# Performance work log

Hardware: AMD Instinct MI355X
Metric: run time of the kernel (lower is better)

The kernel has to match this reference:

```python
import jax, jax.numpy as jnp
import numpy as np

DT = 0.01  # init kwarg dt
M = 501    # microstructure feature length (hardcoded split [501, 501] in source)
H = 128    # hidden width


def _mlp(x, W1, b1, W2, b2):
    # Linear -> Softplus -> Linear
    return jax.nn.softplus(x @ W1 + b1) @ W2 + b2


def _linear_init(key, fan_in, fan_out):
    k1, k2 = jax.random.split(key)
    s = 1.0 / np.sqrt(fan_in)
    W = jax.random.uniform(k1, (fan_in, fan_out), minval=-s, maxval=s, dtype=jnp.float32)
    b = jax.random.uniform(k2, (fan_out,), minval=-s, maxval=s, dtype=jnp.float32)
    return W, b


def setup_inputs() -> dict:
    key = jax.random.key(0)
    ks = jax.random.split(key, 10)
    B, T = 32768, 512
    Ew1, Eb1 = _linear_init(ks[0], 2 * M, H)   # energy net: Linear(1002,128)
    Ew2, Eb2 = _linear_init(ks[1], H, 1)
    nw1, nb1 = _linear_init(ks[2], M, H)       # nu net: Linear(501,128)
    nw2, nb2 = _linear_init(ks[3], H, 1)
    bw1, bb1 = _linear_init(ks[4], 2 * M, H)   # beta net: Linear(1002,128)
    bw2, bb2 = _linear_init(ks[5], H, 1)
    e = jax.random.normal(ks[6], (B, T, 1), dtype=jnp.float32) * 0.01
    e_dot = jax.random.normal(ks[7], (B, T, 1), dtype=jnp.float32) * 0.01
    E = jax.random.uniform(ks[8], (B, M), dtype=jnp.float32)
    nu = jax.random.uniform(ks[9], (B, M), dtype=jnp.float32)
    return dict(e=e, e_dot=e_dot, E=E, nu=nu,
                Ew1=Ew1, Eb1=Eb1, Ew2=Ew2, Eb2=Eb2,
                nw1=nw1, nb1=nb1, nw2=nw2, nb2=nb2,
                bw1=bw1, bb1=bb1, bw2=bw2, bb2=bb2)


def reference(e, e_dot, E, nu,
              Ew1, Eb1, Ew2, Eb2,
              nw1, nb1, nw2, nb2,
              bw1, bb1, bw2, bb2):
    # microstructure encoder: m = concat(E, nu) -> [B, 1002]; constant over time,
    # so the three small MLPs are evaluated ONCE (the per-step autograd.grad of the
    # quadratic energy/dissipation potentials has closed form).
    m = jnp.concatenate((E, nu), axis=-1)
    Emod = jnp.exp(_mlp(m, Ew1, Eb1, Ew2, Eb2))                              # exp(E(m))    [B,1]
    nu_feat = m[:, M:]                                                        # second half of split
    nuv = jnp.exp(jnp.square(_mlp(nu_feat, nw1, nb1, nw2, nb2)) / 40000.0)    # exp(nu(.))   [B,1]
    beta = jnp.square(_mlp(m, bw1, bb1, bw2, bb2)) / 40000.0                  # beta(m)      [B,1]

    # Per-step closed-form derivatives of
    #   energy    = 1/2 exp(E(m)) u^2 + 1/2 (u - v)^2        (u = e_t, v = xi_t)
    #   potential = -1/2 exp(nu) p^2 + 1/2 sum(beta q^2)     (p = e_dot_t, q = -dE/dv = e_t - xi_t)
    #   s_eq = exp(E) u + (u - v);  s_neq = dPhi/dp = -exp(nu) p;  kinetics = dPhi/dq = beta q
    def step(xi, inputs):
        et, edt = inputs                     # [B,1] each
        q = et - xi
        stress_t = Emod * et + q + nuv * edt  # s_eq - s_neq
        xi_next = xi + DT * beta * q
        return xi_next, (stress_t, xi)

    xi0 = jnp.zeros_like(e[:, 0])            # [B,1]
    eT = jnp.moveaxis(e, 1, 0)               # [T,B,1]
    edT = jnp.moveaxis(e_dot, 1, 0)
    _, (stress, xi) = jax.lax.scan(step, xi0, (eT, edT))
    return jnp.moveaxis(stress, 0, 1), jnp.moveaxis(xi, 0, 1)  # [B,T,1] each
```

## Files before the change

### kernel.cpp

```cpp
#include <hip/hip_runtime.h>
#include <hip/hip_bf16.h>

#define M_ 501
#define T_ 512
#define DT_ 0.01f

typedef __attribute__((ext_vector_type(8))) __bf16 bf16x8;
typedef __attribute__((ext_vector_type(4))) float f32x4;

static __device__ __forceinline__ unsigned int pack2(float a, float b) {
    __hip_bfloat16 ha = __float2bfloat16(a);
    __hip_bfloat16 hb = __float2bfloat16(b);
    unsigned short ua = __builtin_bit_cast(unsigned short, ha);
    unsigned short ub = __builtin_bit_cast(unsigned short, hb);
    return (unsigned int)ua | ((unsigned int)ub << 16);
}

__global__ void build_w(const float* __restrict__ Ew1, const float* __restrict__ bw1,
                        const float* __restrict__ nw1, __hip_bfloat16* __restrict__ Wswz) {
    int idx = blockIdx.x * 256 + threadIdx.x;
    if (idx >= 32 * 24 * 64 * 8) return;
    int e  = idx & 7;
    int l  = (idx >> 3) & 63;
    int t  = idx >> 9;
    int nt = t % 24, k0 = t / 24;
    int k  = k0 * 32 + ((l >> 4) << 3) + e;
    int n  = nt * 16 + (l & 15);
    float v = 0.f;
    if (n < 128)      { if (k < 2*M_)             v = Ew1[k * 128 + n]; }
    else if (n < 256) { if (k < 2*M_)             v = bw1[k * 128 + (n - 128)]; }
    else              { if (k >= M_ && k < 2*M_)  v = nw1[(k - M_) * 128 + (n - 256)]; }
    Wswz[idx] = __float2bfloat16(v);
}

__global__ __launch_bounds__(512, 2) void fused_all(
    const float* __restrict__ E, const float* __restrict__ nu,
    const __hip_bfloat16* __restrict__ Wswz,
    const float* __restrict__ Eb1, const float* __restrict__ bb1, const float* __restrict__ nb1,
    const float* __restrict__ Ew2, const float* __restrict__ bw2, const float* __restrict__ nw2,
    const float* __restrict__ Eb2, const float* __restrict__ bb2, const float* __restrict__ nb2,
    const float* __restrict__ e, const float* __restrict__ ed,
    float* __restrict__ stress, float* __restrict__ xiout, int B)
{
    const int tid = threadIdx.x;
    const int wid = tid >> 6, l = tid & 63;
    const int c = l & 15, g = l >> 4;
    const int brow = blockIdx.x * 64;

    __shared__ __align__(16) unsigned char sAraw[3][64 * 128];
    __shared__ float cb1[384], cw2[384];
    __shared__ float lds_s[3][64];

    if (tid < 384) {
        int n = tid;
        cb1[n] = (n < 128) ? Eb1[n] : (n < 256) ? bb1[n - 128] : nb1[n - 256];
        cw2[n] = (n < 128) ? Ew2[n] : (n < 256) ? bw2[n - 128] : nw2[n - 256];
    }
    if (tid < 192) ((float*)lds_s)[tid] = 0.f;

    const int sr = tid >> 3, su = tid & 7;
    const size_t rb = (size_t)(brow + sr) * M_;
    f32x4 qa0, qa1, qa2, qb0, qb1, qb2; int oa = 0, ob = 0;

    auto stage_load = [&](int ch, f32x4& r0, f32x4& r1, f32x4& r2, int& ro) {
        int cu = ch * 8 + su;
        bool slow = (cu == 62) | (cu >= 124);
        if (!slow) {
            const float* src = (cu < 62) ? E : nu;
            int off = (cu < 62) ? cu * 8 : cu * 8 - M_;
            size_t s = rb + (size_t)off;
            ro = (int)(s & 3);
            const f32x4* p = (const f32x4*)(src + (s & ~(size_t)3));
            r0 = p[0]; r1 = p[1]; r2 = p[2];
        } else {
            int kb = cu * 8;
            auto ldx = [&](int k) -> float {
                return (k < M_) ? E[rb + k] : ((k < 2 * M_) ? nu[rb + k - M_] : 0.f);
            };
            r0 = (f32x4){ldx(kb+0), ldx(kb+1), ldx(kb+2), ldx(kb+3)};
            r1 = (f32x4){ldx(kb+4), ldx(kb+5), ldx(kb+6), ldx(kb+7)};
            r2 = (f32x4){0.f, 0.f, 0.f, 0.f};
            ro = 0;
        }
    };
    auto stage_finish = [&](int nbuf, f32x4& r0, f32x4& r1, f32x4& r2, int& ro) {
        asm volatile("" : "+v"(r0), "+v"(r1), "+v"(r2));
        float g0=r0[0], g1=r0[1], g2=r0[2], g3=r0[3],
              g4=r1[0], g5=r1[1], g6=r1[2], g7=r1[3],
              g8=r2[0], g9=r2[1], g10=r2[2];
        const bool o2 = (ro & 2) != 0, o1 = (ro & 1) != 0;
        float u0 = o2?g2:g0, u1 = o2?g3:g1, u2 = o2?g4:g2, u3 = o2?g5:g3,
              u4 = o2?g6:g4, u5 = o2?g7:g5, u6 = o2?g8:g6, u7 = o2?g9:g7,
              u8 = o2?g10:g8;
        float f0 = o1?u1:u0, f1 = o1?u2:u1, f2 = o1?u3:u2, f3 = o1?u4:u3,
              f4 = o1?u5:u4, f5 = o1?u6:u5, f6 = o1?u7:u6, f7 = o1?u8:u7;
        uint4 vv;
        vv.x = pack2(f0, f1); vv.y = pack2(f2, f3);
        vv.z = pack2(f4, f5); vv.w = pack2(f6, f7);
        unsigned bo = ((unsigned)sr << 7) + ((((unsigned)su) << 4) ^ (((unsigned)(sr & 7)) << 4));
        *(uint4*)(sAraw[nbuf] + bo) = vv;
    };

    const bf16x8* wbase = (const bf16x8*)Wswz;

    f32x4 acc[4][3];
    #pragma unroll
    for (int mi = 0; mi < 4; mi++)
        #pragma unroll
        for (int nt = 0; nt < 3; nt++) acc[mi][nt] = (f32x4){0.f, 0.f, 0.f, 0.f};

    auto compute = [&](int bufi, int ch) {
        #pragma unroll
        for (int kk = 0; kk < 2; ++kk) {
            const int kg = ch * 2 + kk;
            bf16x8 w[3];
            #pragma unroll
            for (int nt = 0; nt < 3; ++nt)
                w[nt] = wbase[(size_t)(kg * 24 + wid * 3 + nt) * 64 + l];
            bf16x8 af[4];
            #pragma unroll
            for (int mi = 0; mi < 4; ++mi) {
                int row = c + mi * 16;
                unsigned bo = ((unsigned)row << 7) +
                    ((((unsigned)kk << 6) + ((unsigned)g << 4)) ^ (((unsigned)(row & 7)) << 4));
                af[mi] = *(const bf16x8*)(sAraw[bufi] + bo);
            }
            #pragma unroll
            for (int nt = 0; nt < 3; ++nt)
                #pragma unroll
                for (int mi = 0; mi < 4; ++mi)
                    acc[mi][nt] = __builtin_amdgcn_mfma_f32_16x16x32_bf16(w[nt], af[mi], acc[mi][nt], 0, 0, 0);
        }
    };

    #define BAR() do {                                        \
        asm volatile("s_waitcnt lgkmcnt(0)" ::: "memory");    \
        __builtin_amdgcn_s_barrier();                         \
        __builtin_amdgcn_sched_barrier(0);                    \
    } while (0)

    stage_load(0, qa0, qa1, qa2, oa);
    stage_load(1, qb0, qb1, qb2, ob);
    stage_finish(0, qa0, qa1, qa2, oa);
    stage_load(2, qa0, qa1, qa2, oa);
    stage_finish(1, qb0, qb1, qb2, ob);
    BAR();

    for (int ch = 0; ch < 16; ch += 2) {
        compute(ch % 3, ch);
        if (ch + 3 < 16) stage_load(ch + 3, qb0, qb1, qb2, ob);
        if (ch + 2 < 16) stage_finish((ch + 2) % 3, qa0, qa1, qa2, oa);
        BAR();
        const int c1 = ch + 1;
        compute(c1 % 3, c1);
        if (c1 + 3 < 16) stage_load(c1 + 3, qa0, qa1, qa2, oa);
        if (c1 + 2 < 16) stage_finish((c1 + 2) % 3, qb0, qb1, qb2, ob);
        BAR();
    }
    #undef BAR

    float bv[12], wv[12];
    #pragma unroll
    for (int nt = 0; nt < 3; ++nt)
        #pragma unroll
        for (int r = 0; r < 4; ++r) {
            int nidx = (wid * 3 + nt) * 16 + g * 4 + r;
            bv[nt * 4 + r] = cb1[nidx];
            wv[nt * 4 + r] = cw2[nidx];
        }
    const int m_first = (wid * 3) >> 3, m_last = (wid * 3 + 2) >> 3;

    #pragma unroll
    for (int mi = 0; mi < 4; ++mi) {
        float s0 = 0.f, s1 = 0.f, s2 = 0.f;
        #pragma unroll
        for (int nt = 0; nt < 3; ++nt) {
            float p = 0.f;
            #pragma unroll
            for (int r = 0; r < 4; ++r) {
                float x = acc[mi][nt][r] + bv[nt * 4 + r];
                float h = fmaxf(x, 0.f) + __logf(1.f + __expf(-fabsf(x)));
                p += h * wv[nt * 4 + r];
            }
            int m = (wid * 3 + nt) >> 3;
            if (m == 0) s0 += p; else if (m == 1) s1 += p; else s2 += p;
        }
        auto red = [&](float v, int m) {
            v += __shfl_xor(v, 16);
            v += __shfl_xor(v, 32);
            if (l < 16) atomicAdd(&lds_s[m][mi * 16 + l], v);
        };
        if (m_first == 0) red(s0, 0);
        if (m_first <= 1 && m_last >= 1) red(s1, 1);
        if (m_last == 2) red(s2, 2);
    }
    __syncthreads();

    if (tid < 64) {
        float s0 = lds_s[0][tid], s1 = lds_s[1][tid], s2 = lds_s[2][tid];
        lds_s[0][tid] = __expf(s0 + Eb2[0]);
        float mb = s1 + bb2[0];
        lds_s[1][tid] = mb * mb * (1.f / 40000.f);
        float mn = s2 + nb2[0];
        lds_s[2][tid] = __expf(mn * mn * (1.f / 40000.f));
    }
    __syncthreads();

    for (int i = 0; i < 8; ++i) {
        const int rr = wid * 8 + i;
        const int b = brow + rr;
        float Em = lds_s[0][rr], bt = lds_s[1][rr], nv = lds_s[2][rr];
        float cc = DT_ * bt;
        float a  = 1.f - cc;

        size_t base = (size_t)b * T_ + (size_t)l * 8;
        float4 e0 = *(const float4*)(e + base),  e1 = *(const float4*)(e + base + 4);
        float4 d0 = *(const float4*)(ed + base), d1 = *(const float4*)(ed + base + 4);
        float ev[8] = {e0.x, e0.y, e0.z, e0.w, e1.x, e1.y, e1.z, e1.w};
        float dv[8] = {d0.x, d0.y, d0.z, d0.w, d1.x, d1.y, d1.z, d1.w};

        float S = 0.f;
        #pragma unroll
        for (int j = 0; j < 8; j++) S = a * S + ev[j];
        float a2 = a * a, a4 = a2 * a2, A = a4 * a4;

        #pragma unroll
        for (int d = 1; d < 64; d <<= 1) {
            float Su = __shfl_up(S, d);
            float Au = __shfl_up(A, d);
            if (l >= d) { S = Su * A + S; A = Au * A; }
        }
        float Sp = __shfl_up(S, 1);
        float xi = (l == 0) ? 0.f : cc * Sp;

        float st[8], xo[8];
        #pragma unroll
        for (int j = 0; j < 8; j++) {
            xo[j] = xi;
            float qd = ev[j] - xi;
            st[j] = Em * ev[j] + qd + nv * dv[j];
            xi = xi + cc * qd;
        }
        *(float4*)(stress + base)     = (float4){st[0], st[1], st[2], st[3]};
        *(float4*)(stress + base + 4) = (float4){st[4], st[5], st[6], st[7]};
        *(float4*)(xiout + base)      = (float4){xo[0], xo[1], xo[2], xo[3]};
        *(float4*)(xiout + base + 4)  = (float4){xo[4], xo[5], xo[6], xo[7]};
    }
}

extern "C" void kernel_launch(void* const* d_in, const int* in_sizes, int n_in,
                              void* d_out, int out_size, void* d_ws, size_t ws_size,
                              hipStream_t stream) {
    const float* e   = (const float*)d_in[0];
    const float* ed  = (const float*)d_in[1];
    const float* E   = (const float*)d_in[2];
    const float* nu  = (const float*)d_in[3];
    const float* Ew1 = (const float*)d_in[4];
    const float* Eb1 = (const float*)d_in[5];
    const float* Ew2 = (const float*)d_in[6];
    const float* Eb2 = (const float*)d_in[7];
    const float* nw1 = (const float*)d_in[8];
    const float* nb1 = (const float*)d_in[9];
    const float* nw2 = (const float*)d_in[10];
    const float* nb2 = (const float*)d_in[11];
    const float* bw1 = (const float*)d_in[12];
    const float* bb1 = (const float*)d_in[13];
    const float* bw2 = (const float*)d_in[14];
    const float* bb2 = (const float*)d_in[15];

    int B = in_sizes[2] / M_;

    char* ws = (char*)d_ws;
    __hip_bfloat16* Wswz = (__hip_bfloat16*)ws;

    float* stress = (float*)d_out;
    float* xiout  = stress + (size_t)B * T_;

    build_w<<<(1024 * 384 + 255) / 256, 256, 0, stream>>>(Ew1, bw1, nw1, Wswz);
    fused_all<<<B / 64, 512, 0, stream>>>(E, nu, Wswz, Eb1, bb1, nb1,
                                          Ew2, bw2, nw2, Eb2, bb2, nb2,
                                          e, ed, stress, xiout, B);
}
```

Measured before the change: 136.2 us.

## Swizzle block order, raise MFMA priority, and interleave two rows in scan

```diff
diff --git a/kernel.cpp b/kernel.cpp
--- a/kernel.cpp
+++ b/kernel.cpp
@@ -45,7 +45,9 @@
     const int tid = threadIdx.x;
     const int wid = tid >> 6, l = tid & 63;
     const int c = l & 15, g = l >> 4;
-    const int brow = blockIdx.x * 64;
+    const int bid = blockIdx.x;
+    const int swz = (bid & 7) * 64 + (bid >> 3);
+    const int brow = swz * 64;
 
     __shared__ __align__(16) unsigned char sAraw[3][64 * 128];
     __shared__ float cb1[384], cw2[384];
@@ -125,18 +127,19 @@
                     ((((unsigned)kk << 6) + ((unsigned)g << 4)) ^ (((unsigned)(row & 7)) << 4));
                 af[mi] = *(const bf16x8*)(sAraw[bufi] + bo);
             }
+            __builtin_amdgcn_s_setprio(1);
             #pragma unroll
             for (int nt = 0; nt < 3; ++nt)
                 #pragma unroll
                 for (int mi = 0; mi < 4; ++mi)
                     acc[mi][nt] = __builtin_amdgcn_mfma_f32_16x16x32_bf16(w[nt], af[mi], acc[mi][nt], 0, 0, 0);
+            __builtin_amdgcn_s_setprio(0);
         }
     };
 
     #define BAR() do {                                        \
         asm volatile("s_waitcnt lgkmcnt(0)" ::: "memory");    \
         __builtin_amdgcn_s_barrier();                         \
-        __builtin_amdgcn_sched_barrier(0);                    \
     } while (0)
 
     stage_load(0, qa0, qa1, qa2, oa);
@@ -206,45 +209,60 @@
     }
     __syncthreads();
 
-    for (int i = 0; i < 8; ++i) {
-        const int rr = wid * 8 + i;
-        const int b = brow + rr;
-        float Em = lds_s[0][rr], bt = lds_s[1][rr], nv = lds_s[2][rr];
-        float cc = DT_ * bt;
-        float a  = 1.f - cc;
-
-        size_t base = (size_t)b * T_ + (size_t)l * 8;
-        float4 e0 = *(const float4*)(e + base),  e1 = *(const float4*)(e + base + 4);
-        float4 d0 = *(const float4*)(ed + base), d1 = *(const float4*)(ed + base + 4);
-        float ev[8] = {e0.x, e0.y, e0.z, e0.w, e1.x, e1.y, e1.z, e1.w};
-        float dv[8] = {d0.x, d0.y, d0.z, d0.w, d1.x, d1.y, d1.z, d1.w};
-
-        float S = 0.f;
-        #pragma unroll
-        for (int j = 0; j < 8; j++) S = a * S + ev[j];
-        float a2 = a * a, a4 = a2 * a2, A = a4 * a4;
+    #pragma unroll
+    for (int pi = 0; pi < 4; ++pi) {
+        const int rA = wid * 8 + pi * 2, rB = rA + 1;
+        const int bA = brow + rA, bB = brow + rB;
+        float EmA = lds_s[0][rA], btA = lds_s[1][rA], nvA = lds_s[2][rA];
+        float EmB = lds_s[0][rB], btB = lds_s[1][rB], nvB = lds_s[2][rB];
+        float ccA = DT_ * btA, aA = 1.f - ccA;
+        float ccB = DT_ * btB, aB = 1.f - ccB;
+
+        size_t baA = (size_t)bA * T_ + (size_t)l * 8;
+        size_t baB = (size_t)bB * T_ + (size_t)l * 8;
+        float4 eA0 = *(const float4*)(e + baA),  eA1 = *(const float4*)(e + baA + 4);
+        float4 eB0 = *(const float4*)(e + baB),  eB1 = *(const float4*)(e + baB + 4);
+        float4 dA0 = *(const float4*)(ed + baA), dA1 = *(const float4*)(ed + baA + 4);
+        float4 dB0 = *(const float4*)(ed + baB), dB1 = *(const float4*)(ed + baB + 4);
+        float evA[8] = {eA0.x,eA0.y,eA0.z,eA0.w, eA1.x,eA1.y,eA1.z,eA1.w};
+        float evB[8] = {eB0.x,eB0.y,eB0.z,eB0.w, eB1.x,eB1.y,eB1.z,eB1.w};
+        float dvA[8] = {dA0.x,dA0.y,dA0.z,dA0.w, dA1.x,dA1.y,dA1.z,dA1.w};
+        float dvB[8] = {dB0.x,dB0.y,dB0.z,dB0.w, dB1.x,dB1.y,dB1.z,dB1.w};
+
+        float SA = 0.f, SB = 0.f;
+        #pragma unroll
+        for (int j = 0; j < 8; j++) { SA = aA * SA + evA[j]; SB = aB * SB + evB[j]; }
+        float a2A = aA*aA, AA = (a2A*a2A)*(a2A*a2A);
+        float a2B = aB*aB, AB = (a2B*a2B)*(a2B*a2B);
 
         #pragma unroll
         for (int d = 1; d < 64; d <<= 1) {
-            float Su = __shfl_up(S, d);
-            float Au = __shfl_up(A, d);
-            if (l >= d) { S = Su * A + S; A = Au * A; }
-        }
-        float Sp = __shfl_up(S, 1);
-        float xi = (l == 0) ? 0.f : cc * Sp;
-
-        float st[8], xo[8];
+            float SuA = __shfl_up(SA, d), AuA = __shfl_up(AA, d);
+            float SuB = __shfl_up(SB, d), AuB = __shfl_up(AB, d);
+            if (l >= d) { SA = SuA * AA + SA; AA = AuA * AA;
+                          SB = SuB * AB + SB; AB = AuB * AB; }
+        }
+        float SpA = __shfl_up(SA, 1), SpB = __shfl_up(SB, 1);
+        float xiA = (l == 0) ? 0.f : ccA * SpA;
+        float xiB = (l == 0) ? 0.f : ccB * SpB;
+
+        float stA[8], xoA[8], stB[8], xoB[8];
         #pragma unroll
         for (int j = 0; j < 8; j++) {
-            xo[j] = xi;
-            float qd = ev[j] - xi;
-            st[j] = Em * ev[j] + qd + nv * dv[j];
-            xi = xi + cc * qd;
-        }
-        *(float4*)(stress + base)     = (float4){st[0], st[1], st[2], st[3]};
-        *(float4*)(stress + base + 4) = (float4){st[4], st[5], st[6], st[7]};
-        *(float4*)(xiout + base)      = (float4){xo[0], xo[1], xo[2], xo[3]};
-        *(float4*)(xiout + base + 4)  = (float4){xo[4], xo[5], xo[6], xo[7]};
+            xoA[j] = xiA; xoB[j] = xiB;
+            float qA = evA[j] - xiA, qB = evB[j] - xiB;
+            stA[j] = EmA * evA[j] + qA + nvA * dvA[j];
+            stB[j] = EmB * evB[j] + qB + nvB * dvB[j];
+            xiA += ccA * qA; xiB += ccB * qB;
+        }
+        *(float4*)(stress + baA)     = (float4){stA[0],stA[1],stA[2],stA[3]};
+        *(float4*)(stress + baA + 4) = (float4){stA[4],stA[5],stA[6],stA[7]};
+        *(float4*)(stress + baB)     = (float4){stB[0],stB[1],stB[2],stB[3]};
+        *(float4*)(stress + baB + 4) = (float4){stB[4],stB[5],stB[6],stB[7]};
+        *(float4*)(xiout + baA)      = (float4){xoA[0],xoA[1],xoA[2],xoA[3]};
+        *(float4*)(xiout + baA + 4)  = (float4){xoA[4],xoA[5],xoA[6],xoA[7]};
+        *(float4*)(xiout + baB)      = (float4){xoB[0],xoB[1],xoB[2],xoB[3]};
+        *(float4*)(xiout + baB + 4)  = (float4){xoB[4],xoB[5],xoB[6],xoB[7]};
     }
 }
 
```

After: 121.8 us. 10.6% less time.
